# Optimization experiments

Hardware: AMD Instinct MI355X
Metric: run time of the kernel (lower is better)

Reference implementation:

```python
import jax, jax.numpy as jnp
import numpy as np

B, N, DIM, HEADS, DH, EDGE, DEPTH, K = 4, 128, 256, 8, 64, 64, 2, 512
INNER = HEADS * DH
SCALE = DH ** -0.5


def _ln(x, g, b, eps=1e-5):
    m = x.mean(-1, keepdims=True)
    v = ((x - m) ** 2).mean(-1, keepdims=True)
    return (x - m) / jnp.sqrt(v + eps) * g + b


def _rotate_half(x):
    # interleaved pairs: (d r) with r=2 -> (-x2, x1)
    xp = x.reshape(x.shape[:-1] + (-1, 2))
    x1, x2 = xp[..., 0], xp[..., 1]
    return jnp.stack((-x2, x1), axis=-1).reshape(x.shape)


def _gated_res(x, res, gw):
    gate = jax.nn.sigmoid(jnp.concatenate((x, res, x - res), axis=-1) @ gw)
    return x * gate + res * (1 - gate)


def forward(nodes, edges, edge_ln_g, edge_ln_b, ln1_g, ln1_b, w_exp, b_exp,
            w_q, b_q, w_kv, b_kv, w_ekv, b_ekv, w_out, b_out, gate1_w,
            ln2_g, ln2_b, w_ff1, b_ff1, w_ff2, b_ff2, gate2_w, codebook):
    b, n = nodes.shape[:2]
    # LayerNorm edges over channel dim: (B,C,N,N) -> (B,N,N,C)
    e = _ln(jnp.transpose(edges, (0, 2, 3, 1)), edge_ln_g, edge_ln_b)
    # rotary frequencies over positions, repeated pairwise -> (1, N, DH)
    inv = 1.0 / (10000.0 ** (jnp.arange(0, DH, 2, dtype=jnp.float32) / DH))
    fr = jnp.repeat(jnp.arange(n, dtype=jnp.float32)[:, None] * inv[None, :], 2, axis=-1)
    cos, sin = jnp.cos(fr)[None], jnp.sin(fr)[None]

    def heads3(t):  # (B,N,H*D) -> (B*H,N,D)
        return t.reshape(b, n, HEADS, DH).transpose(0, 2, 1, 3).reshape(b * HEADS, n, DH)

    for i in range(DEPTH):
        # PreNorm + edge-conditioned attention
        x = _ln(nodes, ln1_g[i], ln1_b[i])
        x = x @ w_exp[i] + b_exp[i]
        q = x @ w_q[i] + b_q[i]
        k, v = jnp.split(x @ w_kv[i] + b_kv[i], 2, axis=-1)
        ekv = e @ w_ekv[i] + b_ekv[i]  # (B,N,N,INNER)
        q, k, v = heads3(q), heads3(k), heads3(v)
        ekv = ekv.reshape(b, n, n, HEADS, DH).transpose(0, 3, 1, 2, 4).reshape(b * HEADS, n, n, DH)
        q = q * cos + _rotate_half(q) * sin
        k = k * cos + _rotate_half(k) * sin
        kk = k[:, None, :, :] + ekv  # (BH, i, j, d)
        vv = v[:, None, :, :] + ekv
        sim = jnp.einsum('bid,bijd->bij', q, kk) * SCALE
        att = jax.nn.softmax(sim, axis=-1)
        out = jnp.einsum('bij,bijd->bid', att, vv)
        out = out.reshape(b, HEADS, n, DH).transpose(0, 2, 1, 3).reshape(b, n, INNER)
        out = out @ w_out[i] + b_out[i]
        nodes = _gated_res(out, nodes, gate1_w[i])
        # PreNorm + FeedForward
        h = _ln(nodes, ln2_g[i], ln2_b[i])
        h = jax.nn.gelu(h @ w_ff1[i] + b_ff1[i], approximate=False) @ w_ff2[i] + b_ff2[i]
        nodes = _gated_res(h, nodes, gate2_w[i])

    # VQ codebook nearest-neighbor lookup with straight-through estimator
    z = nodes.reshape(-1, DIM)
    d = (z * z).sum(-1, keepdims=True) - 2.0 * z @ codebook.T + (codebook * codebook).sum(-1)[None, :]
    idx = jnp.argmin(d, axis=-1)
    zq = codebook[idx].reshape(b, n, DIM)
    return nodes + jax.lax.stop_gradient(zq - nodes)


def setup_inputs() -> dict:
    key = jax.random.key(0)
    ks = jax.random.split(key, 16)
    s = 0.02
    inp = {
        'nodes': jax.random.normal(ks[0], (B, N, DIM), jnp.float32),
        'edges': jax.random.normal(ks[1], (B, EDGE, N, N), jnp.float32),
        'edge_ln_g': jnp.ones((EDGE,), jnp.float32),
        'edge_ln_b': jnp.zeros((EDGE,), jnp.float32),
        'ln1_g': jnp.ones((DEPTH, DIM), jnp.float32),
        'ln1_b': jnp.zeros((DEPTH, DIM), jnp.float32),
        'w_exp': s * jax.random.normal(ks[2], (DEPTH, DIM, INNER), jnp.float32),
        'b_exp': jnp.zeros((DEPTH, INNER), jnp.float32),
        'w_q': s * jax.random.normal(ks[3], (DEPTH, INNER, INNER), jnp.float32),
        'b_q': jnp.zeros((DEPTH, INNER), jnp.float32),
        'w_kv': s * jax.random.normal(ks[4], (DEPTH, INNER, 2 * INNER), jnp.float32),
        'b_kv': jnp.zeros((DEPTH, 2 * INNER), jnp.float32),
        'w_ekv': s * jax.random.normal(ks[5], (DEPTH, EDGE, INNER), jnp.float32),
        'b_ekv': jnp.zeros((DEPTH, INNER), jnp.float32),
        'w_out': s * jax.random.normal(ks[6], (DEPTH, INNER, DIM), jnp.float32),
        'b_out': jnp.zeros((DEPTH, DIM), jnp.float32),
        'gate1_w': s * jax.random.normal(ks[7], (DEPTH, 3 * DIM, 1), jnp.float32),
        'ln2_g': jnp.ones((DEPTH, DIM), jnp.float32),
        'ln2_b': jnp.zeros((DEPTH, DIM), jnp.float32),
        'w_ff1': s * jax.random.normal(ks[8], (DEPTH, DIM, 4 * DIM), jnp.float32),
        'b_ff1': jnp.zeros((DEPTH, 4 * DIM), jnp.float32),
        'w_ff2': s * jax.random.normal(ks[9], (DEPTH, 4 * DIM, DIM), jnp.float32),
        'b_ff2': jnp.zeros((DEPTH, DIM), jnp.float32),
        'gate2_w': s * jax.random.normal(ks[10], (DEPTH, 3 * DIM, 1), jnp.float32),
        'codebook': jax.random.uniform(ks[11], (K, DIM), jnp.float32, -1.0 / K, 1.0 / K),
    }
    return inp


def reference(nodes, edges, edge_ln_g, edge_ln_b, ln1_g, ln1_b, w_exp, b_exp,
              w_q, b_q, w_kv, b_kv, w_ekv, b_ekv, w_out, b_out, gate1_w,
              ln2_g, ln2_b, w_ff1, b_ff1, w_ff2, b_ff2, gate2_w, codebook):
    return forward(nodes, edges, edge_ln_g, edge_ln_b, ln1_g, ln1_b, w_exp, b_exp,
                   w_q, b_q, w_kv, b_kv, w_ekv, b_ekv, w_out, b_out, gate1_w,
                   ln2_g, ln2_b, w_ff1, b_ff1, w_ff2, b_ff2, gate2_w, codebook)
```

## Files before the change

kernel.cpp:

```cpp
#include <hip/hip_runtime.h>
#include <math.h>


#define DEV __device__ __forceinline__

constexpr int Bn = 4, Nn = 128, DIMn = 256, HEADSn = 8, DHn = 64, EDGEn = 64,
              DEPTHn = 2, Kn = 512, INNERn = 512;
constexpr int QKVW = 1536;
constexpr int PART = 131072;

DEV float wave_reduce_sum(float v) {
#pragma unroll
  for (int m = 32; m >= 1; m >>= 1) v += __shfl_xor(v, m);
  return v;
}

DEV float block_reduce_sum_256(float v, float* red) {
  v = wave_reduce_sum(v);
  int tid = threadIdx.x;
  if ((tid & 63) == 0) red[tid >> 6] = v;
  __syncthreads();
  v = red[0] + red[1] + red[2] + red[3];
  __syncthreads();
  return v;
}

DEV float gelu_exact(float x) {
  return 0.5f * x * (1.f + erff(x * 0.70710678118654752f));
}

__global__ __launch_bounds__(256) void prep_kernel(
    const float* __restrict__ edges, const float* __restrict__ eg,
    const float* __restrict__ eb, float* __restrict__ e,
    float* __restrict__ eT, float* __restrict__ cost, float* __restrict__ sint,
    const float* __restrict__ nodes_in, const float* __restrict__ ln1_g,
    const float* __restrict__ ln1_b, float* __restrict__ xln,
    float* __restrict__ nodes, const float* __restrict__ wek,
    const float* __restrict__ w_out, const float* __restrict__ bek,
    const float* __restrict__ b_out, float* __restrict__ W2,
    float* __restrict__ b_out2, const float* __restrict__ w_exp,
    const float* __restrict__ b_exp, const float* __restrict__ w_q,
    const float* __restrict__ b_q, const float* __restrict__ w_kv,
    const float* __restrict__ b_kv, float* __restrict__ WqkvF,
    float* __restrict__ bqkvF) {
  __shared__ __align__(16) float smem[4736];
  int blk = blockIdx.x;
  int tid = threadIdx.x;

  if (blk < 432) {
    int t = blk;
    int l = t / 216, r = t % 216;
    int by = r / 24, bx = r % 24;
    bool biasrow = (by == 8);
    float* As = smem;
    float* Bs = smem + 32 * 34;
    int n0 = bx * 64;
    const float* Aab = w_exp + (size_t)l * 256 * 512 + (size_t)(by * 32) * 512;
    const float* be = b_exp + l * 512;
    const float* Wb;
    int ldw;
    if (n0 < 512) {
      Wb = w_q + (size_t)l * 512 * 512 + n0;
      ldw = 512;
    } else {
      Wb = w_kv + (size_t)l * 512 * 1024 + (n0 - 512);
      ldw = 1024;
    }
    int arow = tid >> 3, acol = (tid & 7) << 2;
    int brow = tid >> 4, bcol = (tid & 15) << 2;
    int tx = tid & 15, ty = tid >> 4;
    auto lda = [&](int kpos) -> float4 {
      return biasrow ? *(const float4*)(be + kpos + acol)
                     : *(const float4*)(Aab + (size_t)arow * 512 + kpos + acol);
    };
    float4 a_nxt = lda(0);
    float4 b0_nxt = *(const float4*)(Wb + (size_t)brow * ldw + bcol);
    float4 b1_nxt = *(const float4*)(Wb + (size_t)(brow + 16) * ldw + bcol);
    float acc[2][4] = {};
    for (int k0 = 0; k0 < 512; k0 += 32) {
      As[(acol + 0) * 34 + arow] = a_nxt.x;
      As[(acol + 1) * 34 + arow] = a_nxt.y;
      As[(acol + 2) * 34 + arow] = a_nxt.z;
      As[(acol + 3) * 34 + arow] = a_nxt.w;
      *(float4*)&Bs[brow * 68 + bcol] = b0_nxt;
      *(float4*)&Bs[(brow + 16) * 68 + bcol] = b1_nxt;
      __syncthreads();
      int kn = k0 + 32;
      if (kn < 512) {
        a_nxt = lda(kn);
        b0_nxt = *(const float4*)(Wb + (size_t)(kn + brow) * ldw + bcol);
        b1_nxt = *(const float4*)(Wb + (size_t)(kn + brow + 16) * ldw + bcol);
      }
#pragma unroll
      for (int kk = 0; kk < 32; ++kk) {
        float2 av = *(const float2*)&As[kk * 34 + ty * 2];
        float4 bv = *(const float4*)&Bs[kk * 68 + tx * 4];
        acc[0][0] += av.x * bv.x;
        acc[0][1] += av.x * bv.y;
        acc[0][2] += av.x * bv.z;
        acc[0][3] += av.x * bv.w;
        acc[1][0] += av.y * bv.x;
        acc[1][1] += av.y * bv.y;
        acc[1][2] += av.y * bv.z;
        acc[1][3] += av.y * bv.w;
      }
      __syncthreads();
    }
    if (!biasrow) {
#pragma unroll
      for (int u = 0; u < 2; ++u) {
        int d = by * 32 + ty * 2 + u;
        float4 o = {acc[u][0], acc[u][1], acc[u][2], acc[u][3]};
        *(float4*)(WqkvF + (size_t)l * 256 * 1536 + (size_t)d * 1536 + n0 +
                   tx * 4) = o;
      }
    } else if (ty == 0) {
#pragma unroll
      for (int w = 0; w < 4; ++w) {
        int n = n0 + tx * 4 + w;
        float bb = (n < 512) ? b_q[l * 512 + n] : b_kv[l * 1024 + (n - 512)];
        bqkvF[l * 1536 + n] = acc[0][w] + bb;
      }
    }
  } else if (blk < 944) {
    float* ets = smem;
    float* redS = smem + 4224;
    float* redQ = smem + 4480;
    int eidx = blk - 432;
    int i = eidx & 127, b = eidx >> 7;
    int j = tid & 127, half = tid >> 7;
    const float* src = edges + (size_t)b * EDGEn * Nn * Nn +
                       (size_t)(half * 32) * (Nn * Nn) + i * Nn + j;
    float vals[32];
    float s = 0.f, q = 0.f;
#pragma unroll
    for (int cc = 0; cc < 32; ++cc) {
      float x = src[(size_t)cc * (Nn * Nn)];
      vals[cc] = x;
      s += x;
      q += x * x;
    }
    redS[tid] = s;
    redQ[tid] = q;
    __syncthreads();
    float ts = redS[j] + redS[j + 128];
    float tq = redQ[j] + redQ[j + 128];
    float m = ts * (1.0f / 64.0f);
    float var = tq * (1.0f / 64.0f) - m * m;
    float inv = 1.f / sqrtf(var + 1e-5f);
    float* dst = e + ((size_t)(b * Nn + i) * EDGEn) * Nn + j;
#pragma unroll
    for (int cc = 0; cc < 32; ++cc) {
      int c = half * 32 + cc;
      float o = (vals[cc] - m) * inv * eg[c] + eb[c];
      vals[cc] = o;
      dst[(size_t)c * Nn] = o;
    }
    float* dstT = eT + ((size_t)(b * Nn + i) * Nn) * EDGEn;
#pragma unroll
    for (int ch = 0; ch < 2; ++ch) {
      __syncthreads();
      if (half == ch) {
#pragma unroll
        for (int cc = 0; cc < 32; ++cc) ets[j * 33 + cc] = vals[cc];
      }
      __syncthreads();
#pragma unroll
      for (int it = 0; it < 4; ++it) {
        int f4 = it * 256 + tid;
        int jj = f4 >> 3, c4 = (f4 & 7) << 2;
        float4 o4 = {ets[jj * 33 + c4], ets[jj * 33 + c4 + 1],
                     ets[jj * 33 + c4 + 2], ets[jj * 33 + c4 + 3]};
        *(float4*)(dstT + (size_t)jj * EDGEn + ch * 32 + c4) = o4;
      }
    }
  } else if (blk < 1008) {
    int t = blk - 944;
    int l = t >> 5, h = (t >> 2) & 7, nt = t & 3;
    float* As = smem;
    float* Bs = smem + 2304;
    const float* wekl = wek + (size_t)l * 64 * 512 + h * 64;
    const float* woutl =
        w_out + (size_t)l * 512 * 256 + (size_t)(h * 64) * 256 + nt * 64;
    int tx = tid & 15, ty = tid >> 4;
    float acc[4][4] = {};
    for (int d0 = 0; d0 < 64; d0 += 32) {
      for (int f = tid; f < 512; f += 256) {
        int c = f >> 3, d4 = (f & 7) << 2;
        *(float4*)&As[c * 36 + d4] =
            *(const float4*)(wekl + (size_t)c * 512 + d0 + d4);
      }
      for (int f = tid; f < 512; f += 256) {
        int dd = f >> 4, n4 = (f & 15) << 2;
        *(float4*)&Bs[dd * 68 + n4] =
            *(const float4*)(woutl + (size_t)(d0 + dd) * 256 + n4);
      }
      __syncthreads();
#pragma unroll
      for (int dd = 0; dd < 32; ++dd) {
        float4 bv = *(const float4*)&Bs[dd * 68 + tx * 4];
#pragma unroll
        for (int u = 0; u < 4; ++u) {
          float a = As[(ty * 4 + u) * 36 + dd];
          acc[u][0] += a * bv.x;
          acc[u][1] += a * bv.y;
          acc[u][2] += a * bv.z;
          acc[u][3] += a * bv.w;
        }
      }
      __syncthreads();
    }
#pragma unroll
    for (int u = 0; u < 4; ++u) {
      float4 o = {acc[u][0], acc[u][1], acc[u][2], acc[u][3]};
      *(float4*)(W2 + (size_t)l * 512 * 256 +
                 (size_t)(h * 64 + ty * 4 + u) * 256 + nt * 64 + tx * 4) = o;
    }
  } else if (blk < 1016) {
    int t = blk - 1008;
    int l = t >> 2, nt = t & 3;
    float* part = smem;
    int nn = tid & 63, kq = tid >> 6;
    const float* wcol = w_out + (size_t)l * 512 * 256 + nt * 64 + nn;
    float acc = 0.f;
    for (int k = kq * 128; k < kq * 128 + 128; ++k)
      acc += bek[l * 512 + k] * wcol[(size_t)k * 256];
    part[tid] = acc;
    __syncthreads();
    if (tid < 64)
      b_out2[l * 256 + nt * 64 + nn] =
          b_out[l * 256 + nt * 64 + nn] + part[nn] + part[64 + nn] +
          part[128 + nn] + part[192 + nn];
  } else if (blk < 1032) {
    int t = (blk - 1016) * 256 + tid;
    if (t < Nn * 32) {
      int n = t >> 5, p = t & 31;
      float inv = powf(10000.f, -(float)(2 * p) / 64.f);
      float fr = (float)n * inv;
      cost[t] = cosf(fr);
      sint[t] = sinf(fr);
    }
  } else {
    float* red = smem;
    int row = blk - 1032;
    float v = nodes_in[(size_t)row * DIMn + tid];
    nodes[(size_t)row * DIMn + tid] = v;
    float m = block_reduce_sum_256(v, red) * (1.0f / 256.0f);
    float d = v - m;
    float var = block_reduce_sum_256(d * d, red) * (1.0f / 256.0f);
    float inv = 1.f / sqrtf(var + 1e-5f);
    xln[(size_t)row * DIMn + tid] = d * inv * ln1_g[tid] + ln1_b[tid];
  }
}

__global__ __launch_bounds__(256) void gemm_kernel(
    const float* __restrict__ A, const float* __restrict__ A2, int aact,
    const float* __restrict__ W1, int N1, const float* __restrict__ b1,
    const float* __restrict__ W2n, int N2, const float* __restrict__ b2,
    const float* __restrict__ Wkb, int Ksplit, float* __restrict__ C, int M,
    int Ntot, int K, int kspan, int act, const float* __restrict__ cost,
    const float* __restrict__ sint, float* __restrict__ kT) {
  __shared__ float As[32][34];
  __shared__ __align__(16) float Bs[32][68];
  int tid = threadIdx.x;
  int bx = blockIdx.x, by = blockIdx.y, zid = blockIdx.z;
  int tx = tid & 15, ty = tid >> 4;
  int arow = tid >> 3, acol = (tid & 7) << 2;
  int brow = tid >> 4, bcol = (tid & 15) << 2;
  int col0 = bx * 64;
  const float* W = W1;
  const float* bias = b1;
  int Nw = N1, wcol = col0;
  if (W2n && col0 >= N1) {
    W = W2n;
    bias = b2;
    Nw = N2;
    wcol = col0 - N1;
  }
  int kb = zid * kspan, kend = kb + kspan;
  const float* arp = A + (size_t)(by * 32 + arow) * K;
  const float* arp2 = A2 ? A2 + (size_t)(by * 32 + arow) * K : nullptr;

  auto load_a = [&](int kpos) -> float4 {
    float4 a = *(const float4*)(arp + kpos + acol);
    if (arp2) {
      float4 a2 = *(const float4*)(arp2 + kpos + acol);
      a.x += a2.x;
      a.y += a2.y;
      a.z += a2.z;
      a.w += a2.w;
    }
    if (aact == 1) {
      a.x = gelu_exact(a.x);
      a.y = gelu_exact(a.y);
      a.z = gelu_exact(a.z);
      a.w = gelu_exact(a.w);
    }
    return a;
  };

  float4 a_nxt = load_a(kb);
  const float* w0p;
  const float* w1p;
  {
    int kr0 = kb + brow, kr1 = kb + brow + 16;
    w0p = (Ksplit && kr0 >= Ksplit)
              ? Wkb + (size_t)(kr0 - Ksplit) * Nw + wcol + bcol
              : W + (size_t)kr0 * Nw + wcol + bcol;
    w1p = (Ksplit && kr1 >= Ksplit)
              ? Wkb + (size_t)(kr1 - Ksplit) * Nw + wcol + bcol
              : W + (size_t)kr1 * Nw + wcol + bcol;
  }
  float4 b0_nxt = *(const float4*)w0p;
  float4 b1_nxt = *(const float4*)w1p;

  float acc[2][4] = {};
  for (int k0 = kb; k0 < kend; k0 += 32) {
    As[acol + 0][arow] = a_nxt.x;
    As[acol + 1][arow] = a_nxt.y;
    As[acol + 2][arow] = a_nxt.z;
    As[acol + 3][arow] = a_nxt.w;
    *(float4*)&Bs[brow][bcol] = b0_nxt;
    *(float4*)&Bs[brow + 16][bcol] = b1_nxt;
    __syncthreads();
    int kn = k0 + 32;
    if (kn < kend) {
      a_nxt = load_a(kn);
      int kr0 = kn + brow, kr1 = kn + brow + 16;
      w0p = (Ksplit && kr0 >= Ksplit)
                ? Wkb + (size_t)(kr0 - Ksplit) * Nw + wcol + bcol
                : W + (size_t)kr0 * Nw + wcol + bcol;
      w1p = (Ksplit && kr1 >= Ksplit)
                ? Wkb + (size_t)(kr1 - Ksplit) * Nw + wcol + bcol
                : W + (size_t)kr1 * Nw + wcol + bcol;
      b0_nxt = *(const float4*)w0p;
      b1_nxt = *(const float4*)w1p;
    }
#pragma unroll
    for (int kk = 0; kk < 32; ++kk) {
      float2 av = *(const float2*)&As[kk][ty * 2];
      float4 bv = *(const float4*)&Bs[kk][tx * 4];
      acc[0][0] += av.x * bv.x;
      acc[0][1] += av.x * bv.y;
      acc[0][2] += av.x * bv.z;
      acc[0][3] += av.x * bv.w;
      acc[1][0] += av.y * bv.x;
      acc[1][1] += av.y * bv.y;
      acc[1][2] += av.y * bv.z;
      acc[1][3] += av.y * bv.w;
    }
    __syncthreads();
  }
  int ccol = wcol + tx * 4;
  bool ksec = (act == 4) && (col0 >= 512) && (col0 < 1024);
  float* trans = (float*)Bs;
  float* Cz = C + (size_t)zid * M * Ntot;
#pragma unroll
  for (int u = 0; u < 2; ++u) {
    int r = by * 32 + ty * 2 + u;
    float o[4];
#pragma unroll
    for (int w = 0; w < 4; ++w)
      o[w] = acc[u][w] + (zid == 0 ? bias[ccol + w] : 0.f);
    if (act == 1) {
#pragma unroll
      for (int w = 0; w < 4; ++w) o[w] = gelu_exact(o[w]);
    } else if (act == 4 && col0 < 1024) {
      int n = r & 127;
      int p0 = (ccol & 63) >> 1;
      float c0 = cost[n * 32 + p0], s0 = sint[n * 32 + p0];
      float c1 = cost[n * 32 + p0 + 1], s1 = sint[n * 32 + p0 + 1];
      float x0 = o[0], x1 = o[1], x2 = o[2], x3 = o[3];
      o[0] = x0 * c0 - x1 * s0;
      o[1] = x1 * c0 + x0 * s0;
      o[2] = x2 * c1 - x3 * s1;
      o[3] = x3 * c1 + x2 * s1;
    }
    if (ksec) {
#pragma unroll
      for (int w = 0; w < 4; ++w) trans[(tx * 4 + w) * 33 + ty * 2 + u] = o[w];
    } else {
      float4 o4 = {o[0], o[1], o[2], o[3]};
      *(float4*)(Cz + (size_t)r * Ntot + col0 + tx * 4) = o4;
    }
  }
  if (ksec) {
    __syncthreads();
    int h = (col0 - 512) >> 6;
    int bb = (by * 32) >> 7;
#pragma unroll
    for (int q = 0; q < 2; ++q) {
      int f4 = tid * 2 + q;
      int dl = f4 >> 3, j4 = (f4 & 7) << 2;
      int jj = (by * 32 + j4) & 127;
      float4 o4 = {trans[dl * 33 + j4], trans[dl * 33 + j4 + 1],
                   trans[dl * 33 + j4 + 2], trans[dl * 33 + j4 + 3]};
      *(float4*)(kT + ((size_t)(bb * 8 + h) * 64 + dl) * 128 + jj) = o4;
    }
  }
}

__global__ __launch_bounds__(128) void attn_kernel(
    const float* __restrict__ qkv, const float* __restrict__ e,
    const float* __restrict__ eT, const float* __restrict__ kT,
    const float* __restrict__ wek, const float* __restrict__ w_out,
    const float* __restrict__ W2, float* __restrict__ proj) {
  __shared__ __align__(16) float qs[256];
  __shared__ __align__(16) float qes[256];
  __shared__ __align__(16) float att[512];
  __shared__ float avh[512];
  __shared__ float aeh[512];
  __shared__ float wekh[64 * 65];
  int blk = blockIdx.x;
  int iq = blk & 31;
  int bh = blk >> 5;
  int h = bh & 7, b = bh >> 3;
  int i0 = iq * 4;
  int row0 = b * 128 + i0;
  int tid = threadIdx.x;

  for (int f = tid; f < 256; f += 128) {
    int ii = f >> 6, d = f & 63;
    qs[f] = qkv[(size_t)(row0 + ii) * QKVW + h * 64 + d];
  }
  for (int f = tid; f < 4096; f += 128) {
    int c = f >> 6, d = f & 63;
    wekh[c * 65 + d] = wek[(size_t)c * INNERn + h * 64 + d];
  }
  __syncthreads();

  for (int f = tid; f < 256; f += 128) {
    int ii = f >> 6, c = f & 63;
    float acc = 0.f;
#pragma unroll
    for (int d = 0; d < 64; ++d) acc += qs[ii * 64 + d] * wekh[c * 65 + d];
    qes[f] = acc;
  }
  __syncthreads();

  int i2 = tid >> 5, j4 = tid & 31;
  float s0 = 0.f, s1 = 0.f, s2 = 0.f, s3 = 0.f;
  {
    const float* ktb = kT + ((size_t)bh * 64) * 128 + j4 * 4;
#pragma unroll
    for (int d4 = 0; d4 < 64; d4 += 4) {
      float4 q4 = *(const float4*)&qs[i2 * 64 + d4];
      float4 k0 = *(const float4*)(ktb + (size_t)(d4 + 0) * 128);
      float4 k1 = *(const float4*)(ktb + (size_t)(d4 + 1) * 128);
      float4 k2 = *(const float4*)(ktb + (size_t)(d4 + 2) * 128);
      float4 k3 = *(const float4*)(ktb + (size_t)(d4 + 3) * 128);
      s0 += q4.x * k0.x + q4.y * k1.x + q4.z * k2.x + q4.w * k3.x;
      s1 += q4.x * k0.y + q4.y * k1.y + q4.z * k2.y + q4.w * k3.y;
      s2 += q4.x * k0.z + q4.y * k1.z + q4.z * k2.z + q4.w * k3.z;
      s3 += q4.x * k0.w + q4.y * k1.w + q4.z * k2.w + q4.w * k3.w;
    }
    const float* eb = e + ((size_t)(row0 + i2) * 64) * 128 + j4 * 4;
#pragma unroll
    for (int c4 = 0; c4 < 64; c4 += 4) {
      float4 qe4 = *(const float4*)&qes[i2 * 64 + c4];
      float4 e0 = *(const float4*)(eb + (size_t)(c4 + 0) * 128);
      float4 e1 = *(const float4*)(eb + (size_t)(c4 + 1) * 128);
      float4 e2 = *(const float4*)(eb + (size_t)(c4 + 2) * 128);
      float4 e3 = *(const float4*)(eb + (size_t)(c4 + 3) * 128);
      s0 += qe4.x * e0.x + qe4.y * e1.x + qe4.z * e2.x + qe4.w * e3.x;
      s1 += qe4.x * e0.y + qe4.y * e1.y + qe4.z * e2.y + qe4.w * e3.y;
      s2 += qe4.x * e0.z + qe4.y * e1.z + qe4.z * e2.z + qe4.w * e3.z;
      s3 += qe4.x * e0.w + qe4.y * e1.w + qe4.z * e2.w + qe4.w * e3.w;
    }
    s0 *= 0.125f;
    s1 *= 0.125f;
    s2 *= 0.125f;
    s3 *= 0.125f;
  }
  {
    float mx = fmaxf(fmaxf(s0, s1), fmaxf(s2, s3));
#pragma unroll
    for (int m = 16; m >= 1; m >>= 1) mx = fmaxf(mx, __shfl_xor(mx, m));
    float p0 = expf(s0 - mx), p1 = expf(s1 - mx), p2 = expf(s2 - mx),
          p3 = expf(s3 - mx);
    float sm = p0 + p1 + p2 + p3;
#pragma unroll
    for (int m = 16; m >= 1; m >>= 1) sm += __shfl_xor(sm, m);
    float inv = 1.f / sm;
    float4 a4 = {p0 * inv, p1 * inv, p2 * inv, p3 * inv};
    *(float4*)&att[i2 * 128 + j4 * 4] = a4;
  }
  __syncthreads();

  {
    int d = tid & 63, half = tid >> 6;
    float av0 = 0.f, av1 = 0.f, av2 = 0.f, av3 = 0.f;
    float ae0 = 0.f, ae1 = 0.f, ae2 = 0.f, ae3 = 0.f;
    const float* vb = qkv + (size_t)(b * 128) * QKVW + 1024 + h * 64 + d;
    const float* etb = eT + ((size_t)row0 * 128) * 64 + d;
    for (int jq = 0; jq < 16; ++jq) {
      int jb = half * 64 + jq * 4;
      float4 a0 = *(const float4*)&att[0 * 128 + jb];
      float4 a1 = *(const float4*)&att[1 * 128 + jb];
      float4 a2 = *(const float4*)&att[2 * 128 + jb];
      float4 a3 = *(const float4*)&att[3 * 128 + jb];
#pragma unroll
      for (int t = 0; t < 4; ++t) {
        int j = jb + t;
        float vv = vb[(size_t)j * QKVW];
        float at0 = ((const float*)&a0)[t];
        float at1 = ((const float*)&a1)[t];
        float at2 = ((const float*)&a2)[t];
        float at3 = ((const float*)&a3)[t];
        av0 += at0 * vv;
        av1 += at1 * vv;
        av2 += at2 * vv;
        av3 += at3 * vv;
        float e0 = etb[(size_t)j * 64];
        float e1 = etb[8192 + (size_t)j * 64];
        float e2 = etb[16384 + (size_t)j * 64];
        float e3 = etb[24576 + (size_t)j * 64];
        ae0 += at0 * e0;
        ae1 += at1 * e1;
        ae2 += at2 * e2;
        ae3 += at3 * e3;
      }
    }
    avh[half * 256 + 0 * 64 + d] = av0;
    avh[half * 256 + 1 * 64 + d] = av1;
    avh[half * 256 + 2 * 64 + d] = av2;
    avh[half * 256 + 3 * 64 + d] = av3;
    aeh[half * 256 + 0 * 64 + d] = ae0;
    aeh[half * 256 + 1 * 64 + d] = ae1;
    aeh[half * 256 + 2 * 64 + d] = ae2;
    aeh[half * 256 + 3 * 64 + d] = ae3;
  }
  __syncthreads();

  for (int f = tid; f < 256; f += 128) {
    int ii = f >> 6, dd = f & 63;
    att[ii * 128 + dd] = avh[ii * 64 + dd] + avh[256 + ii * 64 + dd];
    att[ii * 128 + 64 + dd] = aeh[ii * 64 + dd] + aeh[256 + ii * 64 + dd];
  }
  __syncthreads();

  {
    int rp = tid >> 6, n4 = (tid & 63) << 2;
    int r0 = rp * 2, r1 = rp * 2 + 1;
    float o0[4] = {}, o1[4] = {};
    const float* wo = w_out + (size_t)(h * 64) * 256 + n4;
#pragma unroll 8
    for (int k = 0; k < 64; ++k) {
      float4 w4 = *(const float4*)(wo + (size_t)k * 256);
      float a0 = att[r0 * 128 + k];
      float a1 = att[r1 * 128 + k];
      o0[0] += a0 * w4.x;
      o0[1] += a0 * w4.y;
      o0[2] += a0 * w4.z;
      o0[3] += a0 * w4.w;
      o1[0] += a1 * w4.x;
      o1[1] += a1 * w4.y;
      o1[2] += a1 * w4.z;
      o1[3] += a1 * w4.w;
    }
    const float* w2 = W2 + (size_t)(h * 64) * 256 + n4;
#pragma unroll 8
    for (int k = 0; k < 64; ++k) {
      float4 w4 = *(const float4*)(w2 + (size_t)k * 256);
      float a0 = att[r0 * 128 + 64 + k];
      float a1 = att[r1 * 128 + 64 + k];
      o0[0] += a0 * w4.x;
      o0[1] += a0 * w4.y;
      o0[2] += a0 * w4.z;
      o0[3] += a0 * w4.w;
      o1[0] += a1 * w4.x;
      o1[1] += a1 * w4.y;
      o1[2] += a1 * w4.z;
      o1[3] += a1 * w4.w;
    }
    float* pp = proj + (size_t)h * PART;
    float4 v0 = {o0[0], o0[1], o0[2], o0[3]};
    float4 v1 = {o1[0], o1[1], o1[2], o1[3]};
    *(float4*)(pp + (size_t)(row0 + r0) * 256 + n4) = v0;
    *(float4*)(pp + (size_t)(row0 + r1) * 256 + n4) = v1;
  }
}

__global__ __launch_bounds__(256) void gate_ln_kernel(
    const float* __restrict__ x, int nparts, const float* __restrict__ badd,
    float* __restrict__ nodes, const float* __restrict__ gw,
    const float* __restrict__ lng, const float* __restrict__ lnb,
    float* __restrict__ xln) {
  __shared__ float red[4];
  int row = blockIdx.x, tid = threadIdx.x;
  size_t off = (size_t)row * DIMn + tid;
  float xv = x[off];
  for (int p = 1; p < nparts; ++p) xv += x[off + (size_t)p * PART];
  if (badd) xv += badd[tid];
  float rv = nodes[off];
  float pv =
      xv * gw[tid] + rv * gw[DIMn + tid] + (xv - rv) * gw[2 * DIMn + tid];
  float ssum = block_reduce_sum_256(pv, red);
  float gsig = 1.f / (1.f + expf(-ssum));
  float nv = xv * gsig + rv * (1.f - gsig);
  nodes[off] = nv;
  if (lng) {
    float m = block_reduce_sum_256(nv, red) * (1.0f / 256.0f);
    float d = nv - m;
    float var = block_reduce_sum_256(d * d, red) * (1.0f / 256.0f);
    float inv = 1.f / sqrtf(var + 1e-5f);
    xln[off] = d * inv * lng[tid] + lnb[tid];
  }
}

__global__ __launch_bounds__(256) void vq_kernel(
    const float* __restrict__ nodes, const float* __restrict__ codebook,
    float* __restrict__ out) {
  __shared__ __align__(16) float zs[4 * 256];
  __shared__ float wval[4][4];
  __shared__ int widx[4][4];
  __shared__ int fidx[4];
  int row0 = blockIdx.x * 4;
  int tid = threadIdx.x;
  for (int f = tid; f < 1024; f += 256) zs[f] = nodes[(size_t)row0 * DIMn + f];
  __syncthreads();
  int k1 = tid, k2 = tid + 256;
  const float4* c1p = (const float4*)(codebook + (size_t)k1 * DIMn);
  const float4* c2p = (const float4*)(codebook + (size_t)k2 * DIMn);
  float dot[4][2] = {};
  float cc0 = 0.f, cc1 = 0.f;
#pragma unroll 8
  for (int d4 = 0; d4 < 64; ++d4) {
    float4 c1 = c1p[d4], c2 = c2p[d4];
    cc0 += c1.x * c1.x + c1.y * c1.y + c1.z * c1.z + c1.w * c1.w;
    cc1 += c2.x * c2.x + c2.y * c2.y + c2.z * c2.z + c2.w * c2.w;
#pragma unroll
    for (int r = 0; r < 4; ++r) {
      float4 z = *(const float4*)&zs[r * 256 + d4 * 4];
      dot[r][0] += c1.x * z.x + c1.y * z.y + c1.z * z.z + c1.w * z.w;
      dot[r][1] += c2.x * z.x + c2.y * z.y + c2.z * z.z + c2.w * z.w;
    }
  }
  int lane = tid & 63, w = tid >> 6;
#pragma unroll
  for (int r = 0; r < 4; ++r) {
    float bv = cc0 - 2.f * dot[r][0];
    int bi = k1;
    float v2 = cc1 - 2.f * dot[r][1];
    if (v2 < bv) {
      bv = v2;
      bi = k2;
    }
#pragma unroll
    for (int m = 32; m >= 1; m >>= 1) {
      float ov = __shfl_xor(bv, m);
      int oi = __shfl_xor(bi, m);
      if (ov < bv || (ov == bv && oi < bi)) {
        bv = ov;
        bi = oi;
      }
    }
    if (lane == 0) {
      wval[r][w] = bv;
      widx[r][w] = bi;
    }
  }
  __syncthreads();
  if (tid < 4) {
    float bb = wval[tid][0];
    int bi = widx[tid][0];
    for (int t = 1; t < 4; ++t)
      if (wval[tid][t] < bb || (wval[tid][t] == bb && widx[tid][t] < bi)) {
        bb = wval[tid][t];
        bi = widx[tid][t];
      }
    fidx[tid] = bi;
  }
  __syncthreads();
  for (int f = tid; f < 1024; f += 256) {
    int r = f >> 8, d = f & 255;
    float zv = zs[f];
    float zq = codebook[(size_t)fidx[r] * DIMn + d];
    out[(size_t)(row0 + r) * DIMn + d] = zv + (zq - zv);
  }
}

extern "C" void kernel_launch(void* const* d_in, const int* in_sizes, int n_in,
                              void* d_out, int out_size, void* d_ws,
                              size_t ws_size, hipStream_t stream) {
  const float* nodes_in = (const float*)d_in[0];
  const float* edges = (const float*)d_in[1];
  const float* edge_ln_g = (const float*)d_in[2];
  const float* edge_ln_b = (const float*)d_in[3];
  const float* ln1_g = (const float*)d_in[4];
  const float* ln1_b = (const float*)d_in[5];
  const float* w_exp = (const float*)d_in[6];
  const float* b_exp = (const float*)d_in[7];
  const float* w_q = (const float*)d_in[8];
  const float* b_q = (const float*)d_in[9];
  const float* w_kv = (const float*)d_in[10];
  const float* b_kv = (const float*)d_in[11];
  const float* w_ekv = (const float*)d_in[12];
  const float* b_ekv = (const float*)d_in[13];
  const float* w_out = (const float*)d_in[14];
  const float* b_out = (const float*)d_in[15];
  const float* gate1_w = (const float*)d_in[16];
  const float* ln2_g = (const float*)d_in[17];
  const float* ln2_b = (const float*)d_in[18];
  const float* w_ff1 = (const float*)d_in[19];
  const float* b_ff1 = (const float*)d_in[20];
  const float* w_ff2 = (const float*)d_in[21];
  const float* b_ff2 = (const float*)d_in[22];
  const float* gate2_w = (const float*)d_in[23];
  const float* codebook = (const float*)d_in[24];

  float* ws = (float*)d_ws;
  float* e_buf = ws;
  float* eT_buf = e_buf + 4194304;
  float* cost = eT_buf + 4194304;
  float* sint = cost + 4096;
  float* nodes = sint + 4096;
  float* xln = nodes + 131072;
  float* qkvb = xln + 131072;
  float* kTb = qkvb + 786432;
  float* proj = kTb + 262144;
  float* ff1 = proj + 1048576;
  float* W2buf = ff1 + 1048576;
  float* bout2 = W2buf + 262144;
  float* WqkvF = bout2 + 512;
  float* bqkvF = WqkvF + 786432;

  prep_kernel<<<1544, 256, 0, stream>>>(
      edges, edge_ln_g, edge_ln_b, e_buf, eT_buf, cost, sint, nodes_in, ln1_g,
      ln1_b, xln, nodes, w_ekv, w_out, b_ekv, b_out, W2buf, bout2, w_exp,
      b_exp, w_q, b_q, w_kv, b_kv, WqkvF, bqkvF);

  for (int l = 0; l < DEPTHn; ++l) {
    gemm_kernel<<<dim3(24, 16, 1), 256, 0, stream>>>(
        xln, nullptr, 0, WqkvF + (size_t)l * 256 * 1536, 1536,
        bqkvF + l * 1536, nullptr, 0, nullptr, nullptr, 0, qkvb, 512, QKVW,
        256, 256, 4, cost, sint, kTb);
    attn_kernel<<<1024, 128, 0, stream>>>(qkvb, e_buf, eT_buf, kTb,
                                          w_ekv + l * 64 * 512,
                                          w_out + l * 512 * 256,
                                          W2buf + l * 512 * 256, proj);
    gate_ln_kernel<<<512, 256, 0, stream>>>(
        proj, 8, bout2 + l * 256, nodes, gate1_w + l * 768, ln2_g + l * 256,
        ln2_b + l * 256, xln);
    gemm_kernel<<<dim3(16, 16, 2), 256, 0, stream>>>(
        xln, nullptr, 0, w_ff1 + l * 256 * 1024, 1024, b_ff1 + l * 1024,
        nullptr, 0, nullptr, nullptr, 0, ff1, 512, 1024, 256, 128, 0, cost,
        sint, nullptr);
    gemm_kernel<<<dim3(4, 16, 4), 256, 0, stream>>>(
        ff1, ff1 + 524288, 1, w_ff2 + l * 1024 * 256, 256, b_ff2 + l * 256,
        nullptr, 0, nullptr, nullptr, 0, proj, 512, 256, 1024, 256, 0, cost,
        sint, nullptr);
    const float* nlng = (l + 1 < DEPTHn) ? ln1_g + (l + 1) * 256 : nullptr;
    const float* nlnb = (l + 1 < DEPTHn) ? ln1_b + (l + 1) * 256 : nullptr;
    gate_ln_kernel<<<512, 256, 0, stream>>>(proj, 4, nullptr, nodes,
                                            gate2_w + l * 768, nlng, nlnb,
                                            xln);
  }
  vq_kernel<<<128, 256, 0, stream>>>(nodes, codebook, (float*)d_out);
}
```

Before: 319.0 us.

## Process two heads per attention block to share edge-tensor loads

Each attention block now handles two heads for the same 4 query rows instead of one. The edge tensors e and eT, which do not depend on the head, are loaded once and used for both heads, cutting global traffic on the largest inputs. The grid halves to 512 blocks while registers and shared memory per block grow, so occupancy and parallelism may drop. The w_ekv projection is also run sequentially for both heads, which adds extra syncs.

```diff
diff --git a/kernel.cpp b/kernel.cpp
--- a/kernel.cpp
+++ b/kernel.cpp
@@ -405,150 +405,191 @@
     const float* __restrict__ eT, const float* __restrict__ kT,
     const float* __restrict__ wek, const float* __restrict__ w_out,
     const float* __restrict__ W2, float* __restrict__ proj) {
-  __shared__ __align__(16) float qs[256];
-  __shared__ __align__(16) float qes[256];
-  __shared__ __align__(16) float att[512];
-  __shared__ float avh[512];
-  __shared__ float aeh[512];
+  __shared__ __align__(16) float qs[2][256];
+  __shared__ __align__(16) float qes[2][256];
+  __shared__ __align__(16) float att[2][512];
+  __shared__ float avh[2][512];
+  __shared__ float aeh[2][512];
   __shared__ float wekh[64 * 65];
   int blk = blockIdx.x;
   int iq = blk & 31;
-  int bh = blk >> 5;
-  int h = bh & 7, b = bh >> 3;
+  int bh2 = blk >> 5;
+  int hp = bh2 & 3, b = bh2 >> 2;
+  int h0 = hp * 2;
   int i0 = iq * 4;
   int row0 = b * 128 + i0;
   int tid = threadIdx.x;
 
-  for (int f = tid; f < 256; f += 128) {
-    int ii = f >> 6, d = f & 63;
-    qs[f] = qkv[(size_t)(row0 + ii) * QKVW + h * 64 + d];
-  }
-  for (int f = tid; f < 4096; f += 128) {
-    int c = f >> 6, d = f & 63;
-    wekh[c * 65 + d] = wek[(size_t)c * INNERn + h * 64 + d];
+  for (int f = tid; f < 512; f += 128) {
+    int hh = f >> 8, ii = (f >> 6) & 3, d = f & 63;
+    qs[hh][ii * 64 + d] =
+        qkv[(size_t)(row0 + ii) * QKVW + (h0 + hh) * 64 + d];
   }
   __syncthreads();
 
-  for (int f = tid; f < 256; f += 128) {
-    int ii = f >> 6, c = f & 63;
-    float acc = 0.f;
-#pragma unroll
-    for (int d = 0; d < 64; ++d) acc += qs[ii * 64 + d] * wekh[c * 65 + d];
-    qes[f] = acc;
-  }
-  __syncthreads();
+#pragma unroll
+  for (int hh = 0; hh < 2; ++hh) {
+    for (int f = tid; f < 4096; f += 128) {
+      int c = f >> 6, d = f & 63;
+      wekh[c * 65 + d] = wek[(size_t)c * INNERn + (h0 + hh) * 64 + d];
+    }
+    __syncthreads();
+    for (int f = tid; f < 256; f += 128) {
+      int ii = f >> 6, c = f & 63;
+      float acc = 0.f;
+#pragma unroll
+      for (int d = 0; d < 64; ++d)
+        acc += qs[hh][ii * 64 + d] * wekh[c * 65 + d];
+      qes[hh][f] = acc;
+    }
+    __syncthreads();
+  }
 
   int i2 = tid >> 5, j4 = tid & 31;
-  float s0 = 0.f, s1 = 0.f, s2 = 0.f, s3 = 0.f;
   {
-    const float* ktb = kT + ((size_t)bh * 64) * 128 + j4 * 4;
+    float s[2][4] = {};
+    const float* ktb0 = kT + (size_t)(b * 8 + h0) * 8192 + j4 * 4;
 #pragma unroll
     for (int d4 = 0; d4 < 64; d4 += 4) {
-      float4 q4 = *(const float4*)&qs[i2 * 64 + d4];
-      float4 k0 = *(const float4*)(ktb + (size_t)(d4 + 0) * 128);
-      float4 k1 = *(const float4*)(ktb + (size_t)(d4 + 1) * 128);
-      float4 k2 = *(const float4*)(ktb + (size_t)(d4 + 2) * 128);
-      float4 k3 = *(const float4*)(ktb + (size_t)(d4 + 3) * 128);
-      s0 += q4.x * k0.x + q4.y * k1.x + q4.z * k2.x + q4.w * k3.x;
-      s1 += q4.x * k0.y + q4.y * k1.y + q4.z * k2.y + q4.w * k3.y;
-      s2 += q4.x * k0.z + q4.y * k1.z + q4.z * k2.z + q4.w * k3.z;
-      s3 += q4.x * k0.w + q4.y * k1.w + q4.z * k2.w + q4.w * k3.w;
-    }
-    const float* eb = e + ((size_t)(row0 + i2) * 64) * 128 + j4 * 4;
+      float4 qa = *(const float4*)&qs[0][i2 * 64 + d4];
+      float4 qb = *(const float4*)&qs[1][i2 * 64 + d4];
+#pragma unroll
+      for (int t = 0; t < 4; ++t) {
+        float4 k0 = *(const float4*)(ktb0 + (size_t)(d4 + t) * 128);
+        float4 k1 = *(const float4*)(ktb0 + 8192 + (size_t)(d4 + t) * 128);
+        float qa_t = ((const float*)&qa)[t];
+        float qb_t = ((const float*)&qb)[t];
+        s[0][0] += qa_t * k0.x;
+        s[0][1] += qa_t * k0.y;
+        s[0][2] += qa_t * k0.z;
+        s[0][3] += qa_t * k0.w;
+        s[1][0] += qb_t * k1.x;
+        s[1][1] += qb_t * k1.y;
+        s[1][2] += qb_t * k1.z;
+        s[1][3] += qb_t * k1.w;
+      }
+    }
+    const float* ebp = e + (size_t)(row0 + i2) * 8192 + j4 * 4;
 #pragma unroll
     for (int c4 = 0; c4 < 64; c4 += 4) {
-      float4 qe4 = *(const float4*)&qes[i2 * 64 + c4];
-      float4 e0 = *(const float4*)(eb + (size_t)(c4 + 0) * 128);
-      float4 e1 = *(const float4*)(eb + (size_t)(c4 + 1) * 128);
-      float4 e2 = *(const float4*)(eb + (size_t)(c4 + 2) * 128);
-      float4 e3 = *(const float4*)(eb + (size_t)(c4 + 3) * 128);
-      s0 += qe4.x * e0.x + qe4.y * e1.x + qe4.z * e2.x + qe4.w * e3.x;
-      s1 += qe4.x * e0.y + qe4.y * e1.y + qe4.z * e2.y + qe4.w * e3.y;
-      s2 += qe4.x * e0.z + qe4.y * e1.z + qe4.z * e2.z + qe4.w * e3.z;
-      s3 += qe4.x * e0.w + qe4.y * e1.w + qe4.z * e2.w + qe4.w * e3.w;
-    }
-    s0 *= 0.125f;
-    s1 *= 0.125f;
-    s2 *= 0.125f;
-    s3 *= 0.125f;
-  }
-  {
-    float mx = fmaxf(fmaxf(s0, s1), fmaxf(s2, s3));
-#pragma unroll
-    for (int m = 16; m >= 1; m >>= 1) mx = fmaxf(mx, __shfl_xor(mx, m));
-    float p0 = expf(s0 - mx), p1 = expf(s1 - mx), p2 = expf(s2 - mx),
-          p3 = expf(s3 - mx);
-    float sm = p0 + p1 + p2 + p3;
-#pragma unroll
-    for (int m = 16; m >= 1; m >>= 1) sm += __shfl_xor(sm, m);
-    float inv = 1.f / sm;
-    float4 a4 = {p0 * inv, p1 * inv, p2 * inv, p3 * inv};
-    *(float4*)&att[i2 * 128 + j4 * 4] = a4;
+      float4 qea = *(const float4*)&qes[0][i2 * 64 + c4];
+      float4 qeb = *(const float4*)&qes[1][i2 * 64 + c4];
+#pragma unroll
+      for (int t = 0; t < 4; ++t) {
+        float4 ev = *(const float4*)(ebp + (size_t)(c4 + t) * 128);
+        float qa_t = ((const float*)&qea)[t];
+        float qb_t = ((const float*)&qeb)[t];
+        s[0][0] += qa_t * ev.x;
+        s[0][1] += qa_t * ev.y;
+        s[0][2] += qa_t * ev.z;
+        s[0][3] += qa_t * ev.w;
+        s[1][0] += qb_t * ev.x;
+        s[1][1] += qb_t * ev.y;
+        s[1][2] += qb_t * ev.z;
+        s[1][3] += qb_t * ev.w;
+      }
+    }
+#pragma unroll
+    for (int hh = 0; hh < 2; ++hh) {
+      float s0 = s[hh][0] * 0.125f, s1 = s[hh][1] * 0.125f,
+            s2 = s[hh][2] * 0.125f, s3 = s[hh][3] * 0.125f;
+      float mx = fmaxf(fmaxf(s0, s1), fmaxf(s2, s3));
+#pragma unroll
+      for (int m = 16; m >= 1; m >>= 1) mx = fmaxf(mx, __shfl_xor(mx, m));
+      float p0 = expf(s0 - mx), p1 = expf(s1 - mx), p2 = expf(s2 - mx),
+            p3 = expf(s3 - mx);
+      float sm = p0 + p1 + p2 + p3;
+#pragma unroll
+      for (int m = 16; m >= 1; m >>= 1) sm += __shfl_xor(sm, m);
+      float inv = 1.f / sm;
+      float4 a4 = {p0 * inv, p1 * inv, p2 * inv, p3 * inv};
+      *(float4*)&att[hh][i2 * 128 + j4 * 4] = a4;
+    }
   }
   __syncthreads();
 
   {
     int d = tid & 63, half = tid >> 6;
-    float av0 = 0.f, av1 = 0.f, av2 = 0.f, av3 = 0.f;
-    float ae0 = 0.f, ae1 = 0.f, ae2 = 0.f, ae3 = 0.f;
-    const float* vb = qkv + (size_t)(b * 128) * QKVW + 1024 + h * 64 + d;
+    float av[2][4] = {}, ae[2][4] = {};
+    const float* vb0 =
+        qkv + (size_t)(b * 128) * QKVW + 1024 + h0 * 64 + d;
     const float* etb = eT + ((size_t)row0 * 128) * 64 + d;
     for (int jq = 0; jq < 16; ++jq) {
       int jb = half * 64 + jq * 4;
-      float4 a0 = *(const float4*)&att[0 * 128 + jb];
-      float4 a1 = *(const float4*)&att[1 * 128 + jb];
-      float4 a2 = *(const float4*)&att[2 * 128 + jb];
-      float4 a3 = *(const float4*)&att[3 * 128 + jb];
+      float4 a00 = *(const float4*)&att[0][0 * 128 + jb];
+      float4 a01 = *(const float4*)&att[0][1 * 128 + jb];
+      float4 a02 = *(const float4*)&att[0][2 * 128 + jb];
+      float4 a03 = *(const float4*)&att[0][3 * 128 + jb];
+      float4 a10 = *(const float4*)&att[1][0 * 128 + jb];
+      float4 a11 = *(const float4*)&att[1][1 * 128 + jb];
+      float4 a12 = *(const float4*)&att[1][2 * 128 + jb];
+      float4 a13 = *(const float4*)&att[1][3 * 128 + jb];
 #pragma unroll
       for (int t = 0; t < 4; ++t) {
         int j = jb + t;
-        float vv = vb[(size_t)j * QKVW];
-        float at0 = ((const float*)&a0)[t];
-        float at1 = ((const float*)&a1)[t];
-        float at2 = ((const float*)&a2)[t];
-        float at3 = ((const float*)&a3)[t];
-        av0 += at0 * vv;
-        av1 += at1 * vv;
-        av2 += at2 * vv;
-        av3 += at3 * vv;
+        float v0 = vb0[(size_t)j * QKVW];
+        float v1 = vb0[(size_t)j * QKVW + 64];
         float e0 = etb[(size_t)j * 64];
         float e1 = etb[8192 + (size_t)j * 64];
         float e2 = etb[16384 + (size_t)j * 64];
         float e3 = etb[24576 + (size_t)j * 64];
-        ae0 += at0 * e0;
-        ae1 += at1 * e1;
-        ae2 += at2 * e2;
-        ae3 += at3 * e3;
-      }
-    }
-    avh[half * 256 + 0 * 64 + d] = av0;
-    avh[half * 256 + 1 * 64 + d] = av1;
-    avh[half * 256 + 2 * 64 + d] = av2;
-    avh[half * 256 + 3 * 64 + d] = av3;
-    aeh[half * 256 + 0 * 64 + d] = ae0;
-    aeh[half * 256 + 1 * 64 + d] = ae1;
-    aeh[half * 256 + 2 * 64 + d] = ae2;
-    aeh[half * 256 + 3 * 64 + d] = ae3;
+        float a0t0 = ((const float*)&a00)[t];
+        float a0t1 = ((const float*)&a01)[t];
+        float a0t2 = ((const float*)&a02)[t];
+        float a0t3 = ((const float*)&a03)[t];
+        float a1t0 = ((const float*)&a10)[t];
+        float a1t1 = ((const float*)&a11)[t];
+        float a1t2 = ((const float*)&a12)[t];
+        float a1t3 = ((const float*)&a13)[t];
+        av[0][0] += a0t0 * v0;
+        av[0][1] += a0t1 * v0;
+        av[0][2] += a0t2 * v0;
+        av[0][3] += a0t3 * v0;
+        av[1][0] += a1t0 * v1;
+        av[1][1] += a1t1 * v1;
+        av[1][2] += a1t2 * v1;
+        av[1][3] += a1t3 * v1;
+        ae[0][0] += a0t0 * e0;
+        ae[0][1] += a0t1 * e1;
+        ae[0][2] += a0t2 * e2;
+        ae[0][3] += a0t3 * e3;
+        ae[1][0] += a1t0 * e0;
+        ae[1][1] += a1t1 * e1;
+        ae[1][2] += a1t2 * e2;
+        ae[1][3] += a1t3 * e3;
+      }
+    }
+#pragma unroll
+    for (int hh = 0; hh < 2; ++hh) {
+#pragma unroll
+      for (int r = 0; r < 4; ++r) {
+        avh[hh][half * 256 + r * 64 + d] = av[hh][r];
+        aeh[hh][half * 256 + r * 64 + d] = ae[hh][r];
+      }
+    }
   }
   __syncthreads();
 
-  for (int f = tid; f < 256; f += 128) {
-    int ii = f >> 6, dd = f & 63;
-    att[ii * 128 + dd] = avh[ii * 64 + dd] + avh[256 + ii * 64 + dd];
-    att[ii * 128 + 64 + dd] = aeh[ii * 64 + dd] + aeh[256 + ii * 64 + dd];
+  for (int f = tid; f < 512; f += 128) {
+    int hh = f >> 8, ii = (f >> 6) & 3, dd = f & 63;
+    att[hh][ii * 128 + dd] =
+        avh[hh][ii * 64 + dd] + avh[hh][256 + ii * 64 + dd];
+    att[hh][ii * 128 + 64 + dd] =
+        aeh[hh][ii * 64 + dd] + aeh[hh][256 + ii * 64 + dd];
   }
   __syncthreads();
 
-  {
+#pragma unroll
+  for (int hh = 0; hh < 2; ++hh) {
     int rp = tid >> 6, n4 = (tid & 63) << 2;
     int r0 = rp * 2, r1 = rp * 2 + 1;
     float o0[4] = {}, o1[4] = {};
-    const float* wo = w_out + (size_t)(h * 64) * 256 + n4;
+    const float* wo = w_out + (size_t)((h0 + hh) * 64) * 256 + n4;
 #pragma unroll 8
     for (int k = 0; k < 64; ++k) {
       float4 w4 = *(const float4*)(wo + (size_t)k * 256);
-      float a0 = att[r0 * 128 + k];
-      float a1 = att[r1 * 128 + k];
+      float a0 = att[hh][r0 * 128 + k];
+      float a1 = att[hh][r1 * 128 + k];
       o0[0] += a0 * w4.x;
       o0[1] += a0 * w4.y;
       o0[2] += a0 * w4.z;
@@ -558,12 +599,12 @@
       o1[2] += a1 * w4.z;
       o1[3] += a1 * w4.w;
     }
-    const float* w2 = W2 + (size_t)(h * 64) * 256 + n4;
+    const float* w2 = W2 + (size_t)((h0 + hh) * 64) * 256 + n4;
 #pragma unroll 8
     for (int k = 0; k < 64; ++k) {
       float4 w4 = *(const float4*)(w2 + (size_t)k * 256);
-      float a0 = att[r0 * 128 + 64 + k];
-      float a1 = att[r1 * 128 + 64 + k];
+      float a0 = att[hh][r0 * 128 + 64 + k];
+      float a1 = att[hh][r1 * 128 + 64 + k];
       o0[0] += a0 * w4.x;
       o0[1] += a0 * w4.y;
       o0[2] += a0 * w4.z;
@@ -573,7 +614,7 @@
       o1[2] += a1 * w4.z;
       o1[3] += a1 * w4.w;
     }
-    float* pp = proj + (size_t)h * PART;
+    float* pp = proj + (size_t)(h0 + hh) * PART;
     float4 v0 = {o0[0], o0[1], o0[2], o0[3]};
     float4 v1 = {o1[0], o1[1], o1[2], o1[3]};
     *(float4*)(pp + (size_t)(row0 + r0) * 256 + n4) = v0;
@@ -735,10 +776,10 @@
         xln, nullptr, 0, WqkvF + (size_t)l * 256 * 1536, 1536,
         bqkvF + l * 1536, nullptr, 0, nullptr, nullptr, 0, qkvb, 512, QKVW,
         256, 256, 4, cost, sint, kTb);
-    attn_kernel<<<1024, 128, 0, stream>>>(qkvb, e_buf, eT_buf, kTb,
-                                          w_ekv + l * 64 * 512,
-                                          w_out + l * 512 * 256,
-                                          W2buf + l * 512 * 256, proj);
+    attn_kernel<<<512, 128, 0, stream>>>(qkvb, e_buf, eT_buf, kTb,
+                                         w_ekv + l * 64 * 512,
+                                         w_out + l * 512 * 256,
+                                         W2buf + l * 512 * 256, proj);
     gate_ln_kernel<<<512, 256, 0, stream>>>(
         proj, 8, bout2 + l * 256, nodes, gate1_w + l * 768, ln2_g + l * 256,
         ln2_b + l * 256, xln);
```

New measurement: 327.7 us. 2.7% more time.
